# Kernel tuning notes

Hardware: AMD Instinct MI355X
Metric: run time of the kernel (lower is better)

Reference implementation:

```python
import jax, jax.numpy as jnp
import numpy as np

B, T, TC = 128, 300, 20          # batch, words per sentence, chars per word
DW, DC = 16, 32                  # word / char embedding dims
UC, UM = 32, 64                  # char-LSTM units, main-LSTM units
POS, PAR = 20, 8                 # extra feature dims
VW, VC = 1834, 132               # vocab sizes
DIN = DW + UC + POS + PAR        # 76, input dim of main BiLSTM


def setup_inputs() -> dict:
    key = jax.random.key(0)
    ks = jax.random.split(key, 16)
    s = 0.05
    f32 = jnp.float32
    return dict(
        word_in=jax.random.randint(ks[0], (B, T), 0, VW, dtype=jnp.int32),
        char_in=jax.random.randint(ks[1], (B, T, TC), 0, VC, dtype=jnp.int32),
        input_pos=jax.random.normal(ks[2], (B, T, POS), f32),
        input_par=jax.random.normal(ks[3], (B, T, PAR), f32),
        emb_wor=jax.random.normal(ks[4], (VW, DW), f32) * s,
        emb_char=jax.random.normal(ks[5], (VC, DC), f32) * s,
        char_Wx=jax.random.normal(ks[6], (DC, 4 * UC), f32) * s,
        char_Wh=jax.random.normal(ks[7], (UC, 4 * UC), f32) * s,
        char_b=jnp.zeros((4 * UC,), f32),
        fwd_Wx=jax.random.normal(ks[8], (DIN, 4 * UM), f32) * s,
        fwd_Wh=jax.random.normal(ks[9], (UM, 4 * UM), f32) * s,
        fwd_b=jnp.zeros((4 * UM,), f32),
        bwd_Wx=jax.random.normal(ks[10], (DIN, 4 * UM), f32) * s,
        bwd_Wh=jax.random.normal(ks[11], (UM, 4 * UM), f32) * s,
        bwd_b=jnp.zeros((4 * UM,), f32),
        dense_W=jax.random.normal(ks[12], (2 * UM, 4), f32) * s,
        dense_b=jnp.zeros((4,), f32),
    )


def _lstm(x, mask, Wx, Wh, b):
    """Masked Keras-style LSTM (gate order i,f,g,o). x:(N,S,D) mask:(N,S) bool.
    Masked steps carry state (Keras mask_zero semantics). Returns (N,S,U)."""
    U = Wh.shape[0]
    xz = jnp.einsum('nsd,df->nsf', x, Wx) + b  # hoist input projection out of scan

    def step(carry, inp):
        h, c = carry
        z_x, m = inp
        z = z_x + h @ Wh
        i, f, g, o = jnp.split(z, 4, axis=-1)
        c_new = jax.nn.sigmoid(f) * c + jax.nn.sigmoid(i) * jnp.tanh(g)
        h_new = jax.nn.sigmoid(o) * jnp.tanh(c_new)
        m = m[:, None]
        h = jnp.where(m, h_new, h)
        c = jnp.where(m, c_new, c)
        return (h, c), h

    N = x.shape[0]
    h0 = jnp.zeros((N, U), x.dtype)
    (_, _), hs = jax.lax.scan(step, (h0, h0),
                              (jnp.swapaxes(xz, 0, 1), jnp.swapaxes(mask, 0, 1)))
    return jnp.swapaxes(hs, 0, 1)


def reference(word_in, char_in, input_pos, input_par,
              emb_wor, emb_char, char_Wx, char_Wh, char_b,
              fwd_Wx, fwd_Wh, fwd_b, bwd_Wx, bwd_Wh, bwd_b,
              dense_W, dense_b):
    # word embeddings: (B,T,DW)
    ew = emb_wor[word_in]
    # char embeddings, TimeDistributed over words: (B*T, TC, DC)
    ec = emb_char[char_in].reshape(B * T, TC, DC)
    cmask = (char_in != 0).reshape(B * T, TC)
    # char LSTM, return_sequences=False -> final (last-valid) state
    ch = _lstm(ec, cmask, char_Wx, char_Wh, char_b)[:, -1, :].reshape(B, T, UC)
    # concat word emb, char encoding, extra features -> (B,T,DIN)
    x = jnp.concatenate([ew, ch, input_pos, input_par], axis=-1)
    wmask = word_in != 0
    hf = _lstm(x, wmask, fwd_Wx, fwd_Wh, fwd_b)
    hb = _lstm(x[:, ::-1], wmask[:, ::-1], bwd_Wx, bwd_Wh, bwd_b)[:, ::-1]
    h = jnp.concatenate([hf, hb], axis=-1)  # (B,T,2*UM)
    return jax.nn.softmax(h @ dense_W + dense_b, axis=-1)  # (B,T,4)
```

## Files before the change

kernel.cpp:

```cpp
#include <hip/hip_runtime.h>
#include <hip/hip_bf16.h>

#define B_ 128
#define T_ 300
#define TC_ 20
#define DW_ 16
#define DC_ 32
#define UC_ 32
#define UM_ 64
#define POS_ 20
#define PAR_ 8
#define VW_ 1834
#define VC_ 132
#define DIN_ 76
#define XS_ 80
#define NROW (B_*T_)

typedef _Float16 half_t;
typedef half_t h2 __attribute__((ext_vector_type(2)));

__device__ __forceinline__ float fast_sig(float x){
  return __builtin_amdgcn_rcpf(1.f + __expf(-x));
}
__device__ __forceinline__ float fast_tanh(float x){
  return __builtin_amdgcn_rcpf(1.f + __expf(-2.f*x))*2.f - 1.f;
}
__device__ __forceinline__ float dot2u(unsigned int a, unsigned int b, float acc){
  union{unsigned int u; h2 h;} x, y; x.u = a; y.u = b;
#if __has_builtin(__builtin_amdgcn_fdot2)
  return __builtin_amdgcn_fdot2(x.h, y.h, acc, false);
#else
  return acc + (float)x.h.x*(float)y.h.x + (float)x.h.y*(float)y.h.y;
#endif
}
__device__ __forceinline__ float us2f(unsigned short s){
  union{unsigned short s; half_t h;} x; x.s = s; return (float)x.h;
}

__global__ void k_xzc(const float* __restrict__ emb_char, const float* __restrict__ Wx,
                      const float* __restrict__ bias, float* __restrict__ xzc){
  int v = blockIdx.x, j = threadIdx.x;
  float acc = bias[j];
  #pragma unroll
  for (int k=0;k<DC_;k++) acc += emb_char[v*DC_+k]*Wx[k*(4*UC_)+j];
  xzc[v*(4*UC_)+j] = acc;
}

__global__ void k_chT(const float* __restrict__ Wh, half_t* __restrict__ o){
  int t = blockIdx.x*256 + threadIdx.x;
  int j = t >> 5, k = t & 31;
  o[t] = (half_t)Wh[k*(4*UC_)+j];
}

__global__ void k_whT(const float* __restrict__ Whf, const float* __restrict__ Whb,
                      half_t* __restrict__ o){
  int t = blockIdx.x*256 + threadIdx.x;
  int dir = t >> 14;
  int j = (t >> 6) & 255;
  int k = t & 63;
  const float* W = dir ? Whb : Whf;
  o[t] = (half_t)W[k*(4*UM_)+j];
}

__global__ void k_wxT(const float* __restrict__ Wxf, const float* __restrict__ Wxb,
                      half_t* __restrict__ o){
  int t = blockIdx.x*256 + threadIdx.x;
  int dir = t / (256*96);
  int r = t % (256*96);
  int jj = r / 96, k = r % 96;
  const float* W = dir ? Wxb : Wxf;
  o[t] = (k < DIN_) ? (half_t)W[k*(4*UM_)+jj] : (half_t)0.f;
}

__global__ void k_xfill(const int* __restrict__ word_in, const float* __restrict__ emb_wor,
                        const float* __restrict__ pos, const float* __restrict__ par,
                        float* __restrict__ x){
  int r = blockIdx.x*4 + threadIdx.x/80;
  int c = threadIdx.x%80;
  float v;
  if (c < DW_)                     v = emb_wor[word_in[r]*DW_ + c];
  else if (c < DW_+UC_)            return;
  else if (c < DW_+UC_+POS_)       v = pos[r*POS_ + (c-(DW_+UC_))];
  else if (c < DIN_)               v = par[r*PAR_ + (c-(DW_+UC_+POS_))];
  else                             return;
  x[r*XS_ + c] = v;
}

__global__ __launch_bounds__(512,2) void k_char(const int* __restrict__ char_in,
        const float* __restrict__ xzc, const half_t* __restrict__ chT,
        float* __restrict__ x){
  __shared__ unsigned int hbuf2[8][16];
  __shared__ float2 zex[8][64];
  __shared__ int sidx[8*TC_];
  const int tid = threadIdx.x;
  const int w8 = tid >> 6;
  const int lane = tid & 63;
  const int u = lane & 31;
  const int half = lane >> 5;
  const int seq = blockIdx.x*8 + w8;

  if (tid < 8*TC_) sidx[tid] = char_in[blockIdx.x*(8*TC_) + tid];
  if (half==0 && u<16) hbuf2[w8][u] = 0;

  unsigned int wa[16], wb[16];
  {
    const uint4* pa = reinterpret_cast<const uint4*>(chT + (half*64+u)*32);
    const uint4* pb = reinterpret_cast<const uint4*>(chT + (half*64+32+u)*32);
    #pragma unroll
    for (int q=0;q<4;q++){
      uint4 va = pa[q], vb = pb[q];
      wa[q*4+0]=va.x; wa[q*4+1]=va.y; wa[q*4+2]=va.z; wa[q*4+3]=va.w;
      wb[q*4+0]=vb.x; wb[q*4+1]=vb.y; wb[q*4+2]=vb.z; wb[q*4+3]=vb.w;
    }
  }
  __syncthreads();

  float h = 0.f, c = 0.f;
  int idx = sidx[w8*TC_ + 0];
  float za0 = xzc[idx*(4*UC_) + half*64 + u];
  float zb0 = xzc[idx*(4*UC_) + half*64 + 32 + u];

  for (int t=0; t<TC_; t++){
    int idxn = (t+1 < TC_) ? sidx[w8*TC_ + t+1] : 0;
    float zan = xzc[idxn*(4*UC_) + half*64 + u];
    float zbn = xzc[idxn*(4*UC_) + half*64 + 32 + u];

    float za = za0, zb = zb0;
    const uint4* hb = reinterpret_cast<const uint4*>(&hbuf2[w8][0]);
    uint4 q0=hb[0], q1=hb[1], q2=hb[2], q3=hb[3];
    unsigned int hu[16] = {q0.x,q0.y,q0.z,q0.w, q1.x,q1.y,q1.z,q1.w,
                           q2.x,q2.y,q2.z,q2.w, q3.x,q3.y,q3.z,q3.w};
    #pragma unroll
    for (int k=0;k<16;k++){
      za = dot2u(wa[k], hu[k], za);
      zb = dot2u(wb[k], hu[k], zb);
    }
    zex[w8][lane] = make_float2(za, zb);
    if (half == 0){
      float2 p = zex[w8][32+u];
      float zi = za, zf = zb, zg = p.x, zo = p.y;
      float cn = fast_sig(zf)*c + fast_sig(zi)*fast_tanh(zg);
      float hn = fast_sig(zo)*fast_tanh(cn);
      bool m = (idx != 0);
      c = m ? cn : c;
      h = m ? hn : h;
      reinterpret_cast<half_t*>(&hbuf2[w8][0])[u] = (half_t)h;
    }
    idx = idxn; za0 = zan; zb0 = zbn;
  }
  if (half == 0) x[seq*XS_ + DW_ + u] = h;
}

__global__ __launch_bounds__(512,2) void k_xz(const float* __restrict__ x,
      const half_t* __restrict__ wxT_h,
      const float* __restrict__ b_f, const float* __restrict__ b_b,
      half_t* __restrict__ xz){
  __shared__ unsigned int xs[16][40];
  const int j = threadIdx.x;
  const int jj = j & 255;
  const bool bwd = (j >= 256);
  const float bj = bwd ? b_b[jj] : b_f[jj];
  const int u = jj & 63, g = jj >> 6;
  const int ocol = ((bwd ? 4 : 0) + g)*64 + u;

  unsigned int wq[40];
  {
    const uint4* p = reinterpret_cast<const uint4*>(wxT_h + (size_t)((bwd?256:0)+jj)*96);
    #pragma unroll
    for (int q=0;q<10;q++){
      uint4 v = p[q];
      wq[q*4+0]=v.x; wq[q*4+1]=v.y; wq[q*4+2]=v.z; wq[q*4+3]=v.w;
    }
  }

  const int rowbase = blockIdx.x*16;
  for (int i=j; i<16*40; i+=512){
    int r = i/40, q = i%40;
    unsigned int pk = 0;
    if (q < 38){
      float v0 = x[(size_t)(rowbase+r)*XS_ + 2*q];
      float v1 = x[(size_t)(rowbase+r)*XS_ + 2*q+1];
      union{h2 h; unsigned int u;} cv; cv.h = h2{(half_t)v0,(half_t)v1};
      pk = cv.u;
    }
    xs[r][q] = pk;
  }
  __syncthreads();

  for (int r=0; r<16; r++){
    const uint4* xr = reinterpret_cast<const uint4*>(&xs[r][0]);
    float acc = bj;
    #pragma unroll
    for (int q=0;q<10;q++){
      uint4 v = xr[q];
      acc = dot2u(wq[q*4+0], v.x, acc);
      acc = dot2u(wq[q*4+1], v.y, acc);
      acc = dot2u(wq[q*4+2], v.z, acc);
      acc = dot2u(wq[q*4+3], v.w, acc);
    }
    xz[(size_t)(rowbase+r)*512 + ocol] = (half_t)acc;
  }
}

__global__ __launch_bounds__(256,1) void k_rnn(const half_t* __restrict__ xz,
      const int* __restrict__ word_in, const half_t* __restrict__ whT_h,
      float* __restrict__ hcat){
  __shared__ float gbuf[2][4][64];
  __shared__ unsigned int hbuf2[4][32];
  __shared__ int wm[T_];
  const int j = threadIdx.x;
  const int w = j >> 6;
  const int l = j & 63;
  const int dir = blockIdx.x & 1;
  const int b = blockIdx.x >> 1;

  unsigned int wt[32];
  {
    const uint4* p = reinterpret_cast<const uint4*>(whT_h + ((size_t)dir*256 + w*64 + l)*64);
    #pragma unroll
    for (int q=0;q<8;q++){
      uint4 v = p[q];
      wt[q*4+0]=v.x; wt[q*4+1]=v.y; wt[q*4+2]=v.z; wt[q*4+3]=v.w;
    }
  }
  for (int t=j; t<T_; t+=256) wm[t] = word_in[b*T_ + (dir ? (T_-1-t) : t)];
  if (l < 32) hbuf2[w][l] = 0;
  __syncthreads();

  float h = 0.f, c_ = 0.f;
  int row0 = b*T_ + (dir ? T_-1 : 0);
  const half_t* xp = xz + (size_t)row0*512 + (dir*4+w)*64 + l;
  const ptrdiff_t dstep = dir ? -512 : 512;
  float* hout = hcat + (size_t)row0*(2*UM_) + dir*UM_ + l;
  const ptrdiff_t hstep = dir ? -(2*UM_) : (2*UM_);

  unsigned short zx0 = *reinterpret_cast<const unsigned short*>(xp);
  unsigned short zx1 = *reinterpret_cast<const unsigned short*>(xp + dstep);

  for (int t=0; t<T_; t++){
    unsigned short zx2 = 0;
    if (t+2 < T_) zx2 = *reinterpret_cast<const unsigned short*>(xp + 2*dstep);

    const uint4* hb = reinterpret_cast<const uint4*>(&hbuf2[w][0]);
    float a0=0.f, a1=0.f;
    #pragma unroll
    for (int q=0;q<8;q++){
      uint4 hv = hb[q];
      a0 = dot2u(wt[q*4+0], hv.x, a0);
      a1 = dot2u(wt[q*4+1], hv.y, a1);
      a0 = dot2u(wt[q*4+2], hv.z, a0);
      a1 = dot2u(wt[q*4+3], hv.w, a1);
    }
    float z = us2f(zx0) + (a0+a1);
    float nl = (w == 2) ? fast_tanh(z) : fast_sig(z);
    gbuf[t&1][w][l] = nl;
    asm volatile("s_waitcnt lgkmcnt(0)" ::: "memory");
    __builtin_amdgcn_s_barrier();
    asm volatile("" ::: "memory");

    float si = gbuf[t&1][0][l];
    float sf = gbuf[t&1][1][l];
    float tg = gbuf[t&1][2][l];
    float so = gbuf[t&1][3][l];
    int mw = wm[t];
    float cn = sf*c_ + si*tg;
    float hn = so*fast_tanh(cn);
    if (mw != 0){ c_ = cn; h = hn; }
    reinterpret_cast<half_t*>(&hbuf2[w][0])[l] = (half_t)h;
    if (w == 0) *hout = h;
    hout += hstep;
    zx0 = zx1; zx1 = zx2; xp += dstep;
  }
}

__global__ void k_dense(const float* __restrict__ hcat, const float* __restrict__ W,
                        const float* __restrict__ bias, float* __restrict__ out){
  int r = blockIdx.x*256 + threadIdx.x;
  const float4* h4 = reinterpret_cast<const float4*>(hcat + (size_t)r*(2*UM_));
  float a0=bias[0], a1=bias[1], a2=bias[2], a3=bias[3];
  #pragma unroll
  for (int k4=0;k4<32;k4++){
    float4 hv = h4[k4];
    float he[4] = {hv.x, hv.y, hv.z, hv.w};
    #pragma unroll
    for (int e=0;e<4;e++){
      int k = k4*4+e;
      a0 += he[e]*W[k*4+0]; a1 += he[e]*W[k*4+1];
      a2 += he[e]*W[k*4+2]; a3 += he[e]*W[k*4+3];
    }
  }
  float mx = fmaxf(fmaxf(a0,a1), fmaxf(a2,a3));
  float e0=__expf(a0-mx), e1=__expf(a1-mx), e2=__expf(a2-mx), e3=__expf(a3-mx);
  float s = __builtin_amdgcn_rcpf(e0+e1+e2+e3);
  out[r*4+0]=e0*s; out[r*4+1]=e1*s; out[r*4+2]=e2*s; out[r*4+3]=e3*s;
}

extern "C" void kernel_launch(void* const* d_in, const int* in_sizes, int n_in,
                              void* d_out, int out_size, void* d_ws, size_t ws_size,
                              hipStream_t stream) {
  const int*   word_in  = (const int*)  d_in[0];
  const int*   char_in  = (const int*)  d_in[1];
  const float* inp_pos  = (const float*)d_in[2];
  const float* inp_par  = (const float*)d_in[3];
  const float* emb_wor  = (const float*)d_in[4];
  const float* emb_char = (const float*)d_in[5];
  const float* char_Wx  = (const float*)d_in[6];
  const float* char_Wh  = (const float*)d_in[7];
  const float* char_b   = (const float*)d_in[8];
  const float* fwd_Wx   = (const float*)d_in[9];
  const float* fwd_Wh   = (const float*)d_in[10];
  const float* fwd_b    = (const float*)d_in[11];
  const float* bwd_Wx   = (const float*)d_in[12];
  const float* bwd_Wh   = (const float*)d_in[13];
  const float* bwd_b    = (const float*)d_in[14];
  const float* dense_W  = (const float*)d_in[15];
  const float* dense_b  = (const float*)d_in[16];
  float* out = (float*)d_out;

  float* xw   = (float*)d_ws;
  float* hcat = xw + (size_t)NROW*XS_;
  float* xzc  = hcat + (size_t)NROW*128;
  float* fp   = xzc + (size_t)VC_*128;
  half_t* chT   = (half_t*)fp;
  half_t* whT_h = chT + 128*32;
  half_t* wxT_h = whT_h + 2*256*64;
  half_t* xzw   = wxT_h + 2*256*96;

  k_xzc  <<<VC_, 4*UC_, 0, stream>>>(emb_char, char_Wx, char_b, xzc);
  k_chT  <<<16, 256, 0, stream>>>(char_Wh, chT);
  k_whT  <<<128, 256, 0, stream>>>(fwd_Wh, bwd_Wh, whT_h);
  k_wxT  <<<192, 256, 0, stream>>>(fwd_Wx, bwd_Wx, wxT_h);
  k_xfill<<<NROW/4, 320, 0, stream>>>(word_in, emb_wor, inp_pos, inp_par, xw);
  k_char <<<NROW/8, 512, 0, stream>>>(char_in, xzc, chT, xw);
  k_xz   <<<NROW/16, 512, 0, stream>>>(xw, wxT_h, fwd_b, bwd_b, xzw);
  k_rnn  <<<2*B_, 256, 0, stream>>>(xzw, word_in, whT_h, hcat);
  k_dense<<<NROW/256, 256, 0, stream>>>(hcat, dense_W, dense_b, out);
}
```

Baseline: 324.5 us.

## Halve main BiLSTM block to two waves, each computing two gates per unit

The main recurrent kernel now runs with 128 threads (two wavefronts) instead of 256, and each thread computes two gate pre-activations using two register-resident weight rows. The xz layout is interleaved per unit (u*4+g) so each thread loads its two gate inputs with one 32-bit load. Each wave exchanges its pair of gate activations through shared memory rather than gathering all four gates. The aim is a cheaper per-step barrier across fewer waves, at the cost of a longer serial dot-product chain per thread.

Result: slower. 331.9 us (+2.3%).

```diff
diff --git a/kernel.cpp b/kernel.cpp
--- a/kernel.cpp
+++ b/kernel.cpp
@@ -36,6 +36,9 @@
 __device__ __forceinline__ float us2f(unsigned short s){
   union{unsigned short s; half_t h;} x; x.s = s; return (float)x.h;
 }
+__device__ __forceinline__ unsigned int packh2(float a, float b){
+  union{h2 h; unsigned int u;} cv; cv.h = h2{(half_t)a,(half_t)b}; return cv.u;
+}
 
 __global__ void k_xzc(const float* __restrict__ emb_char, const float* __restrict__ Wx,
                       const float* __restrict__ bias, float* __restrict__ xzc){
@@ -161,7 +164,7 @@
   const bool bwd = (j >= 256);
   const float bj = bwd ? b_b[jj] : b_f[jj];
   const int u = jj & 63, g = jj >> 6;
-  const int ocol = ((bwd ? 4 : 0) + g)*64 + u;
+  const int ocol = (bwd ? 256 : 0) + u*4 + g;
 
   unsigned int wq[40];
   {
@@ -180,8 +183,7 @@
     if (q < 38){
       float v0 = x[(size_t)(rowbase+r)*XS_ + 2*q];
       float v1 = x[(size_t)(rowbase+r)*XS_ + 2*q+1];
-      union{h2 h; unsigned int u;} cv; cv.h = h2{(half_t)v0,(half_t)v1};
-      pk = cv.u;
+      pk = packh2(v0, v1);
     }
     xs[r][q] = pk;
   }
@@ -202,11 +204,11 @@
   }
 }
 
-__global__ __launch_bounds__(256,1) void k_rnn(const half_t* __restrict__ xz,
+__global__ __launch_bounds__(128,1) void k_rnn(const half_t* __restrict__ xz,
       const int* __restrict__ word_in, const half_t* __restrict__ whT_h,
       float* __restrict__ hcat){
-  __shared__ float gbuf[2][4][64];
-  __shared__ unsigned int hbuf2[4][32];
+  __shared__ unsigned int hbuf2[2][32];
+  __shared__ float2 pex[2][2][64];
   __shared__ int wm[T_];
   const int j = threadIdx.x;
   const int w = j >> 6;
@@ -214,54 +216,58 @@
   const int dir = blockIdx.x & 1;
   const int b = blockIdx.x >> 1;
 
-  unsigned int wt[32];
+  unsigned int wA[32], wB[32];
   {
-    const uint4* p = reinterpret_cast<const uint4*>(whT_h + ((size_t)dir*256 + w*64 + l)*64);
+    const uint4* pa = reinterpret_cast<const uint4*>(whT_h + ((size_t)dir*256 + (2*w)*64 + l)*64);
+    const uint4* pb = reinterpret_cast<const uint4*>(whT_h + ((size_t)dir*256 + (2*w+1)*64 + l)*64);
     #pragma unroll
     for (int q=0;q<8;q++){
-      uint4 v = p[q];
-      wt[q*4+0]=v.x; wt[q*4+1]=v.y; wt[q*4+2]=v.z; wt[q*4+3]=v.w;
-    }
-  }
-  for (int t=j; t<T_; t+=256) wm[t] = word_in[b*T_ + (dir ? (T_-1-t) : t)];
+      uint4 va = pa[q], vb = pb[q];
+      wA[q*4+0]=va.x; wA[q*4+1]=va.y; wA[q*4+2]=va.z; wA[q*4+3]=va.w;
+      wB[q*4+0]=vb.x; wB[q*4+1]=vb.y; wB[q*4+2]=vb.z; wB[q*4+3]=vb.w;
+    }
+  }
+  for (int t=j; t<T_; t+=128) wm[t] = word_in[b*T_ + (dir ? (T_-1-t) : t)];
   if (l < 32) hbuf2[w][l] = 0;
   __syncthreads();
 
   float h = 0.f, c_ = 0.f;
   int row0 = b*T_ + (dir ? T_-1 : 0);
-  const half_t* xp = xz + (size_t)row0*512 + (dir*4+w)*64 + l;
+  const half_t* xp = xz + (size_t)row0*512 + dir*256 + l*4 + 2*w;
   const ptrdiff_t dstep = dir ? -512 : 512;
   float* hout = hcat + (size_t)row0*(2*UM_) + dir*UM_ + l;
   const ptrdiff_t hstep = dir ? -(2*UM_) : (2*UM_);
 
-  unsigned short zx0 = *reinterpret_cast<const unsigned short*>(xp);
-  unsigned short zx1 = *reinterpret_cast<const unsigned short*>(xp + dstep);
+  ushort2 z0 = *reinterpret_cast<const ushort2*>(xp);
+  ushort2 z1 = *reinterpret_cast<const ushort2*>(xp + dstep);
 
   for (int t=0; t<T_; t++){
-    unsigned short zx2 = 0;
-    if (t+2 < T_) zx2 = *reinterpret_cast<const unsigned short*>(xp + 2*dstep);
+    ushort2 z2 = {0,0};
+    if (t+2 < T_) z2 = *reinterpret_cast<const ushort2*>(xp + 2*dstep);
 
     const uint4* hb = reinterpret_cast<const uint4*>(&hbuf2[w][0]);
-    float a0=0.f, a1=0.f;
+    float aA0=0.f, aA1=0.f, aB0=0.f, aB1=0.f;
     #pragma unroll
     for (int q=0;q<8;q++){
       uint4 hv = hb[q];
-      a0 = dot2u(wt[q*4+0], hv.x, a0);
-      a1 = dot2u(wt[q*4+1], hv.y, a1);
-      a0 = dot2u(wt[q*4+2], hv.z, a0);
-      a1 = dot2u(wt[q*4+3], hv.w, a1);
-    }
-    float z = us2f(zx0) + (a0+a1);
-    float nl = (w == 2) ? fast_tanh(z) : fast_sig(z);
-    gbuf[t&1][w][l] = nl;
+      aA0 = dot2u(wA[q*4+0], hv.x, aA0); aA1 = dot2u(wA[q*4+1], hv.y, aA1);
+      aA0 = dot2u(wA[q*4+2], hv.z, aA0); aA1 = dot2u(wA[q*4+3], hv.w, aA1);
+      aB0 = dot2u(wB[q*4+0], hv.x, aB0); aB1 = dot2u(wB[q*4+1], hv.y, aB1);
+      aB0 = dot2u(wB[q*4+2], hv.z, aB0); aB1 = dot2u(wB[q*4+3], hv.w, aB1);
+    }
+    float zA = us2f(z0.x) + (aA0+aA1);
+    float zB = us2f(z0.y) + (aB0+aB1);
+    float nA = (w == 1) ? fast_tanh(zA) : fast_sig(zA);
+    float nB = fast_sig(zB);
+    pex[t&1][w][l] = make_float2(nA, nB);
     asm volatile("s_waitcnt lgkmcnt(0)" ::: "memory");
     __builtin_amdgcn_s_barrier();
     asm volatile("" ::: "memory");
-
-    float si = gbuf[t&1][0][l];
-    float sf = gbuf[t&1][1][l];
-    float tg = gbuf[t&1][2][l];
-    float so = gbuf[t&1][3][l];
+    float2 p = pex[t&1][1-w][l];
+
+    float si, sf, tg, so;
+    if (w == 0){ si = nA; sf = nB; tg = p.x; so = p.y; }
+    else       { si = p.x; sf = p.y; tg = nA; so = nB; }
     int mw = wm[t];
     float cn = sf*c_ + si*tg;
     float hn = so*fast_tanh(cn);
@@ -269,7 +275,7 @@
     reinterpret_cast<half_t*>(&hbuf2[w][0])[l] = (half_t)h;
     if (w == 0) *hout = h;
     hout += hstep;
-    zx0 = zx1; zx1 = zx2; xp += dstep;
+    z0 = z1; z1 = z2; xp += dstep;
   }
 }
 
@@ -333,6 +339,6 @@
   k_xfill<<<NROW/4, 320, 0, stream>>>(word_in, emb_wor, inp_pos, inp_par, xw);
   k_char <<<NROW/8, 512, 0, stream>>>(char_in, xzc, chT, xw);
   k_xz   <<<NROW/16, 512, 0, stream>>>(xw, wxT_h, fwd_b, bwd_b, xzw);
-  k_rnn  <<<2*B_, 256, 0, stream>>>(xzw, word_in, whT_h, hcat);
+  k_rnn  <<<2*B_, 128, 0, stream>>>(xzw, word_in, whT_h, hcat);
   k_dense<<<NROW/256, 256, 0, stream>>>(hcat, dense_W, dense_b, out);
 }
```
